# Performance work log

Measured on AMD Instinct MI355X. Metric: run time of the kernel, lower is better.

Reference implementation:

```python
import jax, jax.numpy as jnp
import numpy as np

CUBE_SIZE = 3
RADIUS = 0.25
NSAMPLE = 512
B, N = 128, 8192


def make_centers():
    # grid of cube_size^3 centers, centered at origin, spacing = radius
    g = np.arange(CUBE_SIZE, dtype=np.float32)
    c = np.stack(np.meshgrid(g, g, g, indexing='ij'), axis=-1).reshape(-1, 3)
    c -= (CUBE_SIZE - 1) / 2.0
    c *= RADIUS
    return jnp.asarray(c[None])  # [1, P, 3]


def setup_inputs() -> dict:
    key = jax.random.key(0)
    xyz = jax.random.normal(key, (B, N, 3), dtype=jnp.float32)
    return {"xyz": xyz, "centers": make_centers()}


def reference(xyz, centers):
    # xyz: [B, N, 3], centers: [1, P, 3]
    b_, n_, _ = xyz.shape
    p_ = centers.shape[1]
    c = jnp.broadcast_to(centers, (b_, p_, 3))

    # squared distances [B, P, N] without materializing [B,P,N,3]
    x2 = jnp.sum(xyz * xyz, axis=-1)            # [B, N]
    c2 = jnp.sum(c * c, axis=-1)                # [B, P]
    xc = jnp.einsum('bpd,bnd->bpn', c, xyz)     # [B, P, N]
    dist2 = x2[:, None, :] + c2[:, :, None] - 2.0 * xc

    # ball query: first NSAMPLE points (in index order) with dist2 < r^2;
    # remaining slots padded with the first found index (0 if none found),
    # matching the PointNet++ CUDA kernel semantics.
    mask = dist2 < (RADIUS * RADIUS)
    order = jnp.where(mask, jnp.cumsum(mask, axis=-1) - 1, NSAMPLE)  # slot per point
    first_idx = jnp.argmax(mask, axis=-1)                             # [B, P], 0 if none
    idx = jnp.broadcast_to(first_idx[..., None], (b_, p_, NSAMPLE))
    bi = jnp.arange(b_)[:, None, None]
    pi = jnp.arange(p_)[None, :, None]
    js = jnp.broadcast_to(jnp.arange(n_)[None, None, :], (b_, p_, n_))
    idx = idx.at[bi, pi, order].set(js, mode='drop')                  # [B, P, NSAMPLE]

    # gather neighbors and re-center (QueryAndGroup with use_xyz, no features)
    grouped = jnp.take_along_axis(xyz[:, None, :, :], idx[..., None], axis=2)  # [B,P,S,3]
    grouped = grouped - c[:, :, None, :]

    # permute(0,2,3,1) of [B,3,P,S] -> [B,P,S,3] then merge batch and center dims
    return grouped.reshape(b_ * p_, NSAMPLE, 3)
```

## Files before the change

### kernel.cpp

```cpp
#include <hip/hip_runtime.h>


constexpr int P   = 27;
constexpr int N   = 8192;
constexpr int S   = 512;
constexpr int B   = 128;
constexpr int BLK = 256;

__global__ __launch_bounds__(1024) void pc_compact_kernel(
    const float* __restrict__ xyz, float4* __restrict__ cand,
    int* __restrict__ ccnt) {
  int b    = blockIdx.x;
  int tid  = threadIdx.x;
  int lane = tid & 63;
  int wave = tid >> 6;
  __shared__ int s_wsum[16];

  const float4* p4 = (const float4*)(xyz + (size_t)b * (N * 3));
  float4 f[6];
#pragma unroll
  for (int k = 0; k < 6; ++k) f[k] = p4[tid * 6 + k];
  float xs[8], ys[8], zs[8];
  {
    const float* fp = (const float*)f;
#pragma unroll
    for (int k = 0; k < 8; ++k) {
      xs[k] = fp[3 * k + 0]; ys[k] = fp[3 * k + 1]; zs[k] = fp[3 * k + 2];
    }
  }

  unsigned mask = 0;
#pragma unroll
  for (int k = 0; k < 8; ++k) {
    float cx = fminf(fmaxf(roundf(xs[k] * 4.0f), -1.0f), 1.0f) * 0.25f;
    float cy = fminf(fmaxf(roundf(ys[k] * 4.0f), -1.0f), 1.0f) * 0.25f;
    float cz = fminf(fmaxf(roundf(zs[k] * 4.0f), -1.0f), 1.0f) * 0.25f;
    float dx = xs[k] - cx, dy = ys[k] - cy, dz = zs[k] - cz;
    float d2 = dx * dx + dy * dy + dz * dz;
    if (d2 < 0.0625f + 1e-4f) mask |= 1u << k;
  }

  int pcnt = __popc(mask);
  int incl = pcnt;
#pragma unroll
  for (int d = 1; d < 64; d <<= 1) {
    int v = __shfl_up(incl, d);
    if (lane >= d) incl += v;
  }
  if (lane == 63) s_wsum[wave] = incl;
  __syncthreads();
  int woff = 0, total = 0;
#pragma unroll
  for (int w = 0; w < 16; ++w) {
    int c = s_wsum[w];
    if (w < wave) woff += c;
    total += c;
  }
  int pos = woff + (incl - pcnt);

  float4* cb = cand + (size_t)b * N;
#pragma unroll
  for (int k = 0; k < 8; ++k) {
    if (mask & (1u << k)) cb[pos++] = make_float4(xs[k], ys[k], zs[k], 0.0f);
  }
  if (tid == 0) ccnt[b] = total;
}

__global__ __launch_bounds__(BLK) void pc_group2_kernel(
    const float4* __restrict__ cand, const int* __restrict__ ccnt,
    const float* __restrict__ xyz, const float* __restrict__ centers,
    float* __restrict__ out) {
  int i   = blockIdx.x;
  int xcd = i & 7;
  int j   = i >> 3;
  int b   = xcd * 16 + j / P;
  int p   = j - (j / P) * P;

  float cx = centers[p * 3 + 0];
  float cy = centers[p * 3 + 1];
  float cz = centers[p * 3 + 2];
  double cxd = (double)cx, cyd = (double)cy, czd = (double)cz;

  const float4* cb = cand + (size_t)b * N;
  int cnt = ccnt[b];
  float* o = out + ((size_t)b * P + p) * (S * 3);

  __shared__ int   s_wsum[BLK / 64];
  __shared__ float s_first[3];

  int tid  = threadIdx.x;
  int wave = tid >> 6;
  int lane = tid & 63;

  int base = 0;
  for (int start = 0; start < cnt; start += BLK) {
    int idx  = start + tid;
    bool act = idx < cnt;
    float4 pt = make_float4(0.0f, 0.0f, 0.0f, 0.0f);
    if (act) pt = cb[idx];
    double dx = (double)pt.x - cxd;
    double dy = (double)pt.y - cyd;
    double dz = (double)pt.z - czd;
    double d2 = dx * dx + dy * dy + dz * dz;
    bool inball = act && (d2 < 0.0625);

    unsigned long long m = __ballot(inball);
    if (lane == 0) s_wsum[wave] = __popcll(m);
    __syncthreads();

    int woff = 0, total = 0;
#pragma unroll
    for (int w = 0; w < BLK / 64; ++w) {
      int c = s_wsum[w];
      total += c;
      if (w < wave) woff += c;
    }
    int pre  = __popcll(m & ((1ull << lane) - 1ull));
    int slot = base + woff + pre;
    if (inball && slot < S) {
      float fx = pt.x - cx, fy = pt.y - cy, fz = pt.z - cz;
      o[slot * 3 + 0] = fx;
      o[slot * 3 + 1] = fy;
      o[slot * 3 + 2] = fz;
      if (slot == 0) { s_first[0] = fx; s_first[1] = fy; s_first[2] = fz; }
    }
    base += total;
    __syncthreads();
    if (base >= S) break;
  }

  float fx, fy, fz;
  if (base > 0) {
    fx = s_first[0]; fy = s_first[1]; fz = s_first[2];
  } else {
    const float* pts = xyz + (size_t)b * (N * 3);
    fx = pts[0] - cx; fy = pts[1] - cy; fz = pts[2] - cz;
  }
  int filled = base < S ? base : S;
  for (int slot = filled + tid; slot < S; slot += BLK) {
    o[slot * 3 + 0] = fx;
    o[slot * 3 + 1] = fy;
    o[slot * 3 + 2] = fz;
  }
}

__global__ __launch_bounds__(BLK) void pc_group_kernel(
    const float* __restrict__ xyz, const float* __restrict__ centers,
    float* __restrict__ out) {
  int i = blockIdx.x;
  int xcd = i & 7;
  int j = i >> 3;
  int b = xcd * 16 + j / P;
  int p = j - (j / P) * P;

  const float* pts = xyz + (size_t)b * (N * 3);
  float cx = centers[p * 3 + 0];
  float cy = centers[p * 3 + 1];
  float cz = centers[p * 3 + 2];
  double cxd = (double)cx, cyd = (double)cy, czd = (double)cz;
  float* o = out + ((size_t)b * P + p) * (S * 3);

  __shared__ int   s_wavesum[BLK / 64];
  __shared__ float s_first[3];
  int tid = threadIdx.x, wave = tid >> 6, lane = tid & 63;

  int base = 0;
  for (int start = 0; start < N; start += BLK) {
    int n = start + tid;
    float x = pts[n * 3 + 0], y = pts[n * 3 + 1], z = pts[n * 3 + 2];
    double dx = (double)x - cxd, dy = (double)y - cyd, dz = (double)z - czd;
    bool inball = dx * dx + dy * dy + dz * dz < 0.0625;

    unsigned long long m = __ballot(inball);
    if (lane == 0) s_wavesum[wave] = __popcll(m);
    __syncthreads();
    int woff = 0, total = 0;
#pragma unroll
    for (int w = 0; w < BLK / 64; ++w) {
      int c = s_wavesum[w];
      total += c;
      if (w < wave) woff += c;
    }
    int pre = __popcll(m & ((1ull << lane) - 1ull));
    int slot = base + woff + pre;
    if (inball && slot < S) {
      float fx = x - cx, fy = y - cy, fz = z - cz;
      o[slot * 3 + 0] = fx; o[slot * 3 + 1] = fy; o[slot * 3 + 2] = fz;
      if (slot == 0) { s_first[0] = fx; s_first[1] = fy; s_first[2] = fz; }
    }
    base += total;
    __syncthreads();
    if (base >= S) break;
  }
  float fx, fy, fz;
  if (base > 0) { fx = s_first[0]; fy = s_first[1]; fz = s_first[2]; }
  else { fx = pts[0] - cx; fy = pts[1] - cy; fz = pts[2] - cz; }
  int filled = base < S ? base : S;
  for (int slot = filled + tid; slot < S; slot += BLK) {
    o[slot * 3 + 0] = fx; o[slot * 3 + 1] = fy; o[slot * 3 + 2] = fz;
  }
}

extern "C" void kernel_launch(void* const* d_in, const int* in_sizes, int n_in,
                              void* d_out, int out_size, void* d_ws, size_t ws_size,
                              hipStream_t stream) {
  const float* xyz     = (const float*)d_in[0];
  const float* centers = (const float*)d_in[1];
  float* out           = (float*)d_out;

  const size_t cand_bytes = (size_t)B * N * sizeof(float4);
  const size_t need       = cand_bytes + B * sizeof(int);

  if (ws_size >= need) {
    float4* cand = (float4*)d_ws;
    int*    ccnt = (int*)((char*)d_ws + cand_bytes);
    pc_compact_kernel<<<B, 1024, 0, stream>>>(xyz, cand, ccnt);
    pc_group2_kernel<<<B * P, BLK, 0, stream>>>(cand, ccnt, xyz, centers, out);
  } else {
    pc_group_kernel<<<B * P, BLK, 0, stream>>>(xyz, centers, out);
  }
}
```

Measured before the change: 75.32 us.

## Fuse candidate compaction and grouping into one kernel via shared-memory tiles

Replaces the two-kernel pipeline (global candidate compaction, then one block per center scanning candidates) with a single kernel. Each block handles half the centers of one batch and compacts tiles of points into LDS, where one wave per center runs a ballot-based scan. The padding fill now uses float4 stores. This removes the global candidate buffer round trip and one launch. The cost is only 256 blocks of 1024 threads, with waves idle where the center count is under 16, which may underuse the GPU.

```diff
diff --git a/kernel.cpp b/kernel.cpp
--- a/kernel.cpp
+++ b/kernel.cpp
@@ -1,203 +1,169 @@
 #include <hip/hip_runtime.h>
 
 
-constexpr int P   = 27;
-constexpr int N   = 8192;
-constexpr int S   = 512;
-constexpr int B   = 128;
-constexpr int BLK = 256;
+constexpr int P = 27;
+constexpr int N = 8192;
+constexpr int S = 512;
+constexpr int B = 128;
 
-__global__ __launch_bounds__(1024) void pc_compact_kernel(
-    const float* __restrict__ xyz, float4* __restrict__ cand,
-    int* __restrict__ ccnt) {
-  int b    = blockIdx.x;
-  int tid  = threadIdx.x;
-  int lane = tid & 63;
-  int wave = tid >> 6;
-  __shared__ int s_wsum[16];
+constexpr int THREADS = 1024;
+constexpr int TILE    = 4096;
+constexpr int NTILE   = N / TILE;
+constexpr int PT      = TILE / THREADS;
+constexpr int NWAVE   = THREADS / 64;
+constexpr int CPB0    = 14;
 
-  const float4* p4 = (const float4*)(xyz + (size_t)b * (N * 3));
-  float4 f[6];
-#pragma unroll
-  for (int k = 0; k < 6; ++k) f[k] = p4[tid * 6 + k];
-  float xs[8], ys[8], zs[8];
-  {
-    const float* fp = (const float*)f;
-#pragma unroll
-    for (int k = 0; k < 8; ++k) {
-      xs[k] = fp[3 * k + 0]; ys[k] = fp[3 * k + 1]; zs[k] = fp[3 * k + 2];
-    }
-  }
-
-  unsigned mask = 0;
-#pragma unroll
-  for (int k = 0; k < 8; ++k) {
-    float cx = fminf(fmaxf(roundf(xs[k] * 4.0f), -1.0f), 1.0f) * 0.25f;
-    float cy = fminf(fmaxf(roundf(ys[k] * 4.0f), -1.0f), 1.0f) * 0.25f;
-    float cz = fminf(fmaxf(roundf(zs[k] * 4.0f), -1.0f), 1.0f) * 0.25f;
-    float dx = xs[k] - cx, dy = ys[k] - cy, dz = zs[k] - cz;
-    float d2 = dx * dx + dy * dy + dz * dz;
-    if (d2 < 0.0625f + 1e-4f) mask |= 1u << k;
-  }
-
-  int pcnt = __popc(mask);
-  int incl = pcnt;
-#pragma unroll
-  for (int d = 1; d < 64; d <<= 1) {
-    int v = __shfl_up(incl, d);
-    if (lane >= d) incl += v;
-  }
-  if (lane == 63) s_wsum[wave] = incl;
-  __syncthreads();
-  int woff = 0, total = 0;
-#pragma unroll
-  for (int w = 0; w < 16; ++w) {
-    int c = s_wsum[w];
-    if (w < wave) woff += c;
-    total += c;
-  }
-  int pos = woff + (incl - pcnt);
-
-  float4* cb = cand + (size_t)b * N;
-#pragma unroll
-  for (int k = 0; k < 8; ++k) {
-    if (mask & (1u << k)) cb[pos++] = make_float4(xs[k], ys[k], zs[k], 0.0f);
-  }
-  if (tid == 0) ccnt[b] = total;
-}
-
-__global__ __launch_bounds__(BLK) void pc_group2_kernel(
-    const float4* __restrict__ cand, const int* __restrict__ ccnt,
+__global__ __launch_bounds__(THREADS) void pc_fused_kernel(
     const float* __restrict__ xyz, const float* __restrict__ centers,
     float* __restrict__ out) {
-  int i   = blockIdx.x;
-  int xcd = i & 7;
-  int j   = i >> 3;
-  int b   = xcd * 16 + j / P;
-  int p   = j - (j / P) * P;
+  int bid  = blockIdx.x;
+  int xcd  = bid & 7;
+  int j    = bid >> 3;
+  int b    = xcd * 16 + (j >> 1);
+  int half = j & 1;
 
-  float cx = centers[p * 3 + 0];
-  float cy = centers[p * 3 + 1];
-  float cz = centers[p * 3 + 2];
-  double cxd = (double)cx, cyd = (double)cy, czd = (double)cz;
-
-  const float4* cb = cand + (size_t)b * N;
-  int cnt = ccnt[b];
-  float* o = out + ((size_t)b * P + p) * (S * 3);
-
-  __shared__ int   s_wsum[BLK / 64];
-  __shared__ float s_first[3];
+  int cstart = half ? CPB0 : 0;
+  int ccount = half ? (P - CPB0) : CPB0;
 
   int tid  = threadIdx.x;
   int wave = tid >> 6;
   int lane = tid & 63;
 
-  int base = 0;
-  for (int start = 0; start < cnt; start += BLK) {
-    int idx  = start + tid;
-    bool act = idx < cnt;
-    float4 pt = make_float4(0.0f, 0.0f, 0.0f, 0.0f);
-    if (act) pt = cb[idx];
-    double dx = (double)pt.x - cxd;
-    double dy = (double)pt.y - cyd;
-    double dz = (double)pt.z - czd;
-    double d2 = dx * dx + dy * dy + dz * dz;
-    bool inball = act && (d2 < 0.0625);
+  __shared__ float s_x[TILE], s_y[TILE], s_z[TILE];
+  __shared__ int   s_wsum[NWAVE];
 
-    unsigned long long m = __ballot(inball);
-    if (lane == 0) s_wsum[wave] = __popcll(m);
-    __syncthreads();
+  const float4* p4 = (const float4*)(xyz + (size_t)b * (N * 3));
 
-    int woff = 0, total = 0;
+  bool  cw = wave < ccount;
+  int   c  = cstart + (cw ? wave : 0);
+  float cx = 0.0f, cy = 0.0f, cz = 0.0f;
+  if (cw) {
+    cx = centers[c * 3 + 0];
+    cy = centers[c * 3 + 1];
+    cz = centers[c * 3 + 2];
+  }
+  double cxd = (double)cx, cyd = (double)cy, czd = (double)cz;
+  float* o = out + ((size_t)b * P + c) * (S * 3);
+
+  int   cbase = 0;
+  bool  hasf  = false;
+  float f0x = 0.0f, f0y = 0.0f, f0z = 0.0f;
+
+  for (int tile = 0; tile < NTILE; ++tile) {
+    float4 f[3];
+    int fbase = tile * (TILE * 3 / 4) + tid * 3;
 #pragma unroll
-    for (int w = 0; w < BLK / 64; ++w) {
-      int c = s_wsum[w];
-      total += c;
-      if (w < wave) woff += c;
+    for (int k = 0; k < 3; ++k) f[k] = p4[fbase + k];
+    float xs[PT], ys[PT], zs[PT];
+    {
+      const float* fp = (const float*)f;
+#pragma unroll
+      for (int k = 0; k < PT; ++k) {
+        xs[k] = fp[3 * k + 0];
+        ys[k] = fp[3 * k + 1];
+        zs[k] = fp[3 * k + 2];
+      }
     }
-    int pre  = __popcll(m & ((1ull << lane) - 1ull));
-    int slot = base + woff + pre;
-    if (inball && slot < S) {
-      float fx = pt.x - cx, fy = pt.y - cy, fz = pt.z - cz;
-      o[slot * 3 + 0] = fx;
-      o[slot * 3 + 1] = fy;
-      o[slot * 3 + 2] = fz;
-      if (slot == 0) { s_first[0] = fx; s_first[1] = fy; s_first[2] = fz; }
+    unsigned mask = 0;
+#pragma unroll
+    for (int k = 0; k < PT; ++k) {
+      float gx = fminf(fmaxf(roundf(xs[k] * 4.0f), -1.0f), 1.0f) * 0.25f;
+      float gy = fminf(fmaxf(roundf(ys[k] * 4.0f), -1.0f), 1.0f) * 0.25f;
+      float gz = fminf(fmaxf(roundf(zs[k] * 4.0f), -1.0f), 1.0f) * 0.25f;
+      float dx = xs[k] - gx, dy = ys[k] - gy, dz = zs[k] - gz;
+      float d2 = dx * dx + dy * dy + dz * dz;
+      if (d2 < 0.0625f + 1e-4f) mask |= 1u << k;
     }
-    base += total;
-    __syncthreads();
-    if (base >= S) break;
-  }
 
-  float fx, fy, fz;
-  if (base > 0) {
-    fx = s_first[0]; fy = s_first[1]; fz = s_first[2];
-  } else {
-    const float* pts = xyz + (size_t)b * (N * 3);
-    fx = pts[0] - cx; fy = pts[1] - cy; fz = pts[2] - cz;
-  }
-  int filled = base < S ? base : S;
-  for (int slot = filled + tid; slot < S; slot += BLK) {
-    o[slot * 3 + 0] = fx;
-    o[slot * 3 + 1] = fy;
-    o[slot * 3 + 2] = fz;
-  }
-}
-
-__global__ __launch_bounds__(BLK) void pc_group_kernel(
-    const float* __restrict__ xyz, const float* __restrict__ centers,
-    float* __restrict__ out) {
-  int i = blockIdx.x;
-  int xcd = i & 7;
-  int j = i >> 3;
-  int b = xcd * 16 + j / P;
-  int p = j - (j / P) * P;
-
-  const float* pts = xyz + (size_t)b * (N * 3);
-  float cx = centers[p * 3 + 0];
-  float cy = centers[p * 3 + 1];
-  float cz = centers[p * 3 + 2];
-  double cxd = (double)cx, cyd = (double)cy, czd = (double)cz;
-  float* o = out + ((size_t)b * P + p) * (S * 3);
-
-  __shared__ int   s_wavesum[BLK / 64];
-  __shared__ float s_first[3];
-  int tid = threadIdx.x, wave = tid >> 6, lane = tid & 63;
-
-  int base = 0;
-  for (int start = 0; start < N; start += BLK) {
-    int n = start + tid;
-    float x = pts[n * 3 + 0], y = pts[n * 3 + 1], z = pts[n * 3 + 2];
-    double dx = (double)x - cxd, dy = (double)y - cyd, dz = (double)z - czd;
-    bool inball = dx * dx + dy * dy + dz * dz < 0.0625;
-
-    unsigned long long m = __ballot(inball);
-    if (lane == 0) s_wavesum[wave] = __popcll(m);
+    int pcnt = __popc(mask);
+    int incl = pcnt;
+#pragma unroll
+    for (int d = 1; d < 64; d <<= 1) {
+      int v = __shfl_up(incl, d);
+      if (lane >= d) incl += v;
+    }
+    if (lane == 63) s_wsum[wave] = incl;
     __syncthreads();
     int woff = 0, total = 0;
 #pragma unroll
-    for (int w = 0; w < BLK / 64; ++w) {
-      int c = s_wavesum[w];
-      total += c;
-      if (w < wave) woff += c;
+    for (int w = 0; w < NWAVE; ++w) {
+      int cnt = s_wsum[w];
+      total += cnt;
+      if (w < wave) woff += cnt;
     }
-    int pre = __popcll(m & ((1ull << lane) - 1ull));
-    int slot = base + woff + pre;
-    if (inball && slot < S) {
-      float fx = x - cx, fy = y - cy, fz = z - cz;
-      o[slot * 3 + 0] = fx; o[slot * 3 + 1] = fy; o[slot * 3 + 2] = fz;
-      if (slot == 0) { s_first[0] = fx; s_first[1] = fy; s_first[2] = fz; }
+    int pos = woff + (incl - pcnt);
+#pragma unroll
+    for (int k = 0; k < PT; ++k) {
+      if (mask & (1u << k)) {
+        s_x[pos] = xs[k];
+        s_y[pos] = ys[k];
+        s_z[pos] = zs[k];
+        ++pos;
+      }
     }
-    base += total;
     __syncthreads();
-    if (base >= S) break;
+
+    if (cw && cbase < S) {
+      for (int cb0 = 0; cb0 < total; cb0 += 64) {
+        int  i   = cb0 + lane;
+        bool act = i < total;
+        float px = 0.0f, py = 0.0f, pz = 0.0f;
+        if (act) { px = s_x[i]; py = s_y[i]; pz = s_z[i]; }
+        double dx = (double)px - cxd;
+        double dy = (double)py - cyd;
+        double dz = (double)pz - czd;
+        bool inball = act && (dx * dx + dy * dy + dz * dz < 0.0625);
+
+        unsigned long long m = __ballot(inball);
+        int pre  = __popcll(m & ((1ull << lane) - 1ull));
+        int slot = cbase + pre;
+        if (inball && slot < S) {
+          float fx = px - cx, fy = py - cy, fz = pz - cz;
+          o[slot * 3 + 0] = fx;
+          o[slot * 3 + 1] = fy;
+          o[slot * 3 + 2] = fz;
+          if (slot == 0) { hasf = true; f0x = fx; f0y = fy; f0z = fz; }
+        }
+        cbase += __popcll(m);
+        if (cbase >= S) break;
+      }
+    }
+    __syncthreads();
   }
-  float fx, fy, fz;
-  if (base > 0) { fx = s_first[0]; fy = s_first[1]; fz = s_first[2]; }
-  else { fx = pts[0] - cx; fy = pts[1] - cy; fz = pts[2] - cz; }
-  int filled = base < S ? base : S;
-  for (int slot = filled + tid; slot < S; slot += BLK) {
-    o[slot * 3 + 0] = fx; o[slot * 3 + 1] = fy; o[slot * 3 + 2] = fz;
+
+  if (cw) {
+    float fx, fy, fz;
+    if (cbase > 0) {
+      unsigned long long fm = __ballot(hasf);
+      int src = __builtin_ctzll(fm);
+      fx = __shfl(f0x, src);
+      fy = __shfl(f0y, src);
+      fz = __shfl(f0z, src);
+    } else {
+      const float* pts = xyz + (size_t)b * (N * 3);
+      fx = pts[0] - cx;
+      fy = pts[1] - cy;
+      fz = pts[2] - cz;
+    }
+    int filled = cbase < S ? cbase : S;
+    int f0i  = filled * 3;
+    int q0   = (f0i + 3) >> 2;
+    int head = q0 * 4 - f0i;
+    if (head > S * 3 - f0i) head = S * 3 - f0i;
+    if (lane < head) {
+      int idx = f0i + lane;
+      int r   = idx % 3;
+      float val = (r == 0) ? fx : ((r == 1) ? fy : fz);
+      o[idx] = val;
+    }
+    float4* o4 = (float4*)o;
+    for (int q = q0 + lane; q < (S * 3) / 4; q += 64) {
+      int r = q % 3;
+      float a0 = (r == 0) ? fx : ((r == 1) ? fy : fz);
+      float a1 = (r == 0) ? fy : ((r == 1) ? fz : fx);
+      float a2 = (r == 0) ? fz : ((r == 1) ? fx : fy);
+      o4[q] = make_float4(a0, a1, a2, a0);
+    }
   }
 }
 
@@ -207,16 +173,7 @@
   const float* xyz     = (const float*)d_in[0];
   const float* centers = (const float*)d_in[1];
   float* out           = (float*)d_out;
+  (void)d_ws; (void)ws_size;
 
-  const size_t cand_bytes = (size_t)B * N * sizeof(float4);
-  const size_t need       = cand_bytes + B * sizeof(int);
-
-  if (ws_size >= need) {
-    float4* cand = (float4*)d_ws;
-    int*    ccnt = (int*)((char*)d_ws + cand_bytes);
-    pc_compact_kernel<<<B, 1024, 0, stream>>>(xyz, cand, ccnt);
-    pc_group2_kernel<<<B * P, BLK, 0, stream>>>(cand, ccnt, xyz, centers, out);
-  } else {
-    pc_group_kernel<<<B * P, BLK, 0, stream>>>(xyz, centers, out);
-  }
+  pc_fused_kernel<<<B * 2, THREADS, 0, stream>>>(xyz, centers, out);
 }
```

Measured after the change: 75.23 us. No clear change (-0.1%).
